# Optimization experiments

Hardware: AMD Instinct MI355X
Metric: run time of the kernel (lower is better)

## Reference

```python
import jax, jax.numpy as jnp
import numpy as np

V, E, H = 50000, 256, 512
BS, SEQ = 64, 200


def setup_inputs() -> dict:
    key = jax.random.key(0)
    ks = jax.random.split(key, 16)
    s = 0.05
    return {
        "input_idx": jax.random.randint(ks[0], (BS,), 0, V),
        "encoded": jax.random.normal(ks[1], (BS, SEQ, 2 * H), jnp.float32),
        "encoded_idx": jax.random.randint(ks[2], (BS, SEQ), 0, V),
        "prev_state": jax.random.normal(ks[3], (BS, H), jnp.float32),
        "weighted": jax.random.normal(ks[4], (BS, 1, 2 * H), jnp.float32),
        "order": 1,
        "embed_W": jax.random.normal(ks[5], (V, E), jnp.float32) * s,
        "Wih": jax.random.normal(ks[6], (3 * H, E + 2 * H), jnp.float32) * s,
        "Whh": jax.random.normal(ks[7], (3 * H, H), jnp.float32) * s,
        "bih": jax.random.normal(ks[8], (3 * H,), jnp.float32) * s,
        "bhh": jax.random.normal(ks[9], (3 * H,), jnp.float32) * s,
        "Ws_W": jax.random.normal(ks[10], (H, 2 * H), jnp.float32) * s,
        "Ws_b": jax.random.normal(ks[11], (H,), jnp.float32) * s,
        "Wo_W": jax.random.normal(ks[12], (V, H), jnp.float32) * s,
        "Wo_b": jax.random.normal(ks[13], (V,), jnp.float32) * s,
        "Wc_W": jax.random.normal(ks[14], (H, 2 * H), jnp.float32) * s,
        "Wc_b": jax.random.normal(ks[15], (H,), jnp.float32) * s,
    }


def reference(input_idx, encoded, encoded_idx, prev_state, weighted, order,
              embed_W, Wih, Whh, bih, bhh, Ws_W, Ws_b, Wo_W, Wo_b, Wc_W, Wc_b):
    bs, seq, _ = encoded.shape
    hidden = Ws_W.shape[0]
    vocab = Wo_W.shape[0]

    if order == 0:
        prev_state = encoded[:, 1] @ Ws_W.T + Ws_b            # [bs, H]
        weighted = jnp.zeros((bs, 1, 2 * hidden), encoded.dtype)

    # GRU single step (batch_first, seq len 1)
    x = jnp.concatenate([embed_W[input_idx], weighted[:, 0, :]], axis=1)  # [bs, E+2H]
    gi = x @ Wih.T + bih                                       # [bs, 3H]
    gh = prev_state @ Whh.T + bhh                              # [bs, 3H]
    i_r, i_z, i_n = jnp.split(gi, 3, axis=1)
    h_r, h_z, h_n = jnp.split(gh, 3, axis=1)
    r = jax.nn.sigmoid(i_r + h_r)
    z = jax.nn.sigmoid(i_z + h_z)
    n = jnp.tanh(i_n + r * h_n)
    state = (1.0 - z) * n + z * prev_state                     # [bs, H]

    # generate and copy scores
    score_g = state @ Wo_W.T + Wo_b                            # [bs, V]
    sc = jnp.tanh(encoded @ Wc_W.T + Wc_b)                     # [bs, seq, H]
    score_c = jnp.einsum('bsh,bh->bs', sc, state)              # [bs, seq]
    enc_mask = jnp.where(encoded_idx == 0, -1000.0, 0.0).astype(score_c.dtype)
    score_c = jnp.tanh(score_c + enc_mask)

    probs = jax.nn.softmax(jnp.concatenate([score_g, score_c], axis=1), axis=1)
    prob_g = probs[:, :vocab]                                  # [bs, V]
    prob_c = probs[:, vocab:]                                  # [bs, seq]

    # scatter-add copy probs into vocab slots
    prob_c_to_g = jnp.zeros((bs, vocab), probs.dtype).at[
        jnp.arange(bs)[:, None], encoded_idx].add(prob_c)
    out = (prob_g + prob_c_to_g)[:, None, :]                   # [bs, 1, V]

    # selective-read attention over positions matching input token
    m = (encoded_idx == input_idx[:, None]).astype(encoded.dtype)  # [bs, seq]
    ssum = m.sum(axis=1, keepdims=True)
    m = jnp.where(ssum > 1, m / ssum, m)
    attn = (prob_c * m)[:, None, :]                            # [bs, 1, seq]
    weighted_out = attn @ encoded                              # [bs, 1, 2H]

    return out, state, weighted_out
```

## Files before the change

### kernel.cpp

```cpp
#include <hip/hip_runtime.h>

#define V 50000
#define E_DIM 256
#define H_DIM 512
#define H2 1024
#define G3 1536
#define BSZ 64
#define SEQ 200
#define KX 1280
#define MROWS 12800
#define NBLK_WO 391

#define XBF_OFF   0
#define H0_OFF    40960
#define H0BF_OFF  73728
#define GI_OFF    90112
#define GH_OFF    188416
#define STBF_OFF  286720
#define WCBF_OFF  303104
#define SC_OFF    565248
#define REDG_OFF  590848
#define RED_OFF   690944

#define OUT_STATE 3200000
#define OUT_W     3232768

typedef __attribute__((ext_vector_type(8))) short bf16x8;
typedef __attribute__((ext_vector_type(4))) float f32x4;

__device__ __forceinline__ float sigmf(float x) { return 1.f / (1.f + __expf(-x)); }

__device__ __forceinline__ ushort f2bf(float f) {
  uint u = __float_as_uint(f);
  uint r = (u + 0x7FFFu + ((u >> 16) & 1u)) >> 16;
  return (ushort)r;
}

__device__ __forceinline__ float tanhfast(float x) {
  float xc = fminf(15.f, fmaxf(-15.f, x));
  float e = __expf(2.f * xc);
  return (e - 1.f) * __builtin_amdgcn_rcpf(e + 1.f);
}

__device__ __forceinline__ bf16x8 cvt8(float4 a, float4 b) {
  union { bf16x8 v; uint u[4]; } r;
  asm("v_cvt_pk_bf16_f32 %0, %1, %2" : "=v"(r.u[0]) : "v"(a.x), "v"(a.y));
  asm("v_cvt_pk_bf16_f32 %0, %1, %2" : "=v"(r.u[1]) : "v"(a.z), "v"(a.w));
  asm("v_cvt_pk_bf16_f32 %0, %1, %2" : "=v"(r.u[2]) : "v"(b.x), "v"(b.y));
  asm("v_cvt_pk_bf16_f32 %0, %1, %2" : "=v"(r.u[3]) : "v"(b.z), "v"(b.w));
  return r.v;
}

__device__ __forceinline__ void gload16(const void* g, void* l) {
  __builtin_amdgcn_global_load_lds(
      (__attribute__((address_space(1))) void*)(g),
      (__attribute__((address_space(3))) void*)(l), 16, 0, 0);
}

__global__ void kprep(const float* __restrict__ Wc_W, ushort* __restrict__ Wc_bf,
                      const int* __restrict__ input_idx, const float* __restrict__ encoded,
                      const float* __restrict__ prev_state, const float* __restrict__ weighted,
                      const int* __restrict__ order_p, const float* __restrict__ embed_W,
                      const float* __restrict__ Ws_W, const float* __restrict__ Ws_b,
                      ushort* __restrict__ x_bf, float* __restrict__ h0,
                      ushort* __restrict__ h0_bf) {
  int bid = blockIdx.x, tid = threadIdx.x;
  if (bid < 512) {
    int i = bid * 256 + tid;
    float4 v = ((const float4*)Wc_W)[i];
    ushort4 o;
    o.x = f2bf(v.x); o.y = f2bf(v.y); o.z = f2bf(v.z); o.w = f2bf(v.w);
    ((ushort4*)Wc_bf)[i] = o;
    return;
  }
  int b = bid - 512;
  int order = order_p[0];
  int idx = input_idx[b];
  x_bf[b * KX + tid] = f2bf(embed_W[(size_t)idx * E_DIM + tid]);
  if (order != 0) {
    for (int j = tid; j < H2; j += 256) x_bf[b * KX + E_DIM + j] = f2bf(weighted[b * H2 + j]);
    for (int j = tid; j < H_DIM; j += 256) {
      float v = prev_state[b * H_DIM + j];
      h0[b * H_DIM + j] = v;
      h0_bf[b * H_DIM + j] = f2bf(v);
    }
  } else {
    for (int j = tid; j < H2; j += 256) x_bf[b * KX + E_DIM + j] = 0;
    const float* er = encoded + ((size_t)b * SEQ + 1) * H2;
    for (int j = tid; j < H_DIM; j += 256) {
      float acc = Ws_b[j];
      const float* wr = Ws_W + (size_t)j * H2;
      for (int k = 0; k < H2; ++k) acc = fmaf(er[k], wr[k], acc);
      h0[b * H_DIM + j] = acc;
      h0_bf[b * H_DIM + j] = f2bf(acc);
    }
  }
}

__device__ __forceinline__ void gemm_small(const ushort* __restrict__ Abf,
                                           const float* __restrict__ W,
                                           const float* __restrict__ bias,
                                           float* __restrict__ out, int N, int kdim,
                                           int bid) {
  int tid = threadIdx.x;
  int lane = tid & 63, wv = tid >> 6;
  int l15 = lane & 15, lg = lane >> 4;
  int n0 = (bid * 4 + wv) * 16;
  int col = n0 + l15;
  bool valid = col < N;
  int colc = valid ? col : N - 1;
  f32x4 acc[4];
#pragma unroll
  for (int mt = 0; mt < 4; ++mt) acc[mt] = (f32x4){0.f, 0.f, 0.f, 0.f};
  const float* wrow = W + (size_t)colc * kdim + lg * 8;
  const ushort* arow = Abf + (size_t)l15 * kdim + lg * 8;
#pragma unroll 4
  for (int k0 = 0; k0 < kdim; k0 += 32) {
    float4 w0 = *(const float4*)(wrow + k0);
    float4 w1 = *(const float4*)(wrow + k0 + 4);
    bf16x8 bf = cvt8(w0, w1);
#pragma unroll
    for (int mt = 0; mt < 4; ++mt) {
      bf16x8 af = *(const bf16x8*)(arow + (size_t)mt * 16 * kdim + k0);
      acc[mt] = __builtin_amdgcn_mfma_f32_16x16x32_bf16(af, bf, acc[mt], 0, 0, 0);
    }
  }
  float bv = bias[colc];
  if (valid) {
#pragma unroll
    for (int mt = 0; mt < 4; ++mt)
#pragma unroll
      for (int r = 0; r < 4; ++r)
        out[(size_t)(mt * 16 + lg * 4 + r) * N + col] = acc[mt][r] + bv;
  }
}

__global__ __launch_bounds__(256) void mfma_gates(const ushort* __restrict__ x_bf,
                                                  const float* __restrict__ Wih,
                                                  const float* __restrict__ bih,
                                                  const ushort* __restrict__ h0_bf,
                                                  const float* __restrict__ Whh,
                                                  const float* __restrict__ bhh,
                                                  float* __restrict__ gi, float* __restrict__ gh) {
  if (blockIdx.y == 0)
    gemm_small(x_bf, Wih, bih, gi, G3, KX, blockIdx.x);
  else
    gemm_small(h0_bf, Whh, bhh, gh, G3, H_DIM, blockIdx.x);
}

__global__ void k2_gru(const float* __restrict__ gi, const float* __restrict__ gh,
                       const float* __restrict__ h0, float* __restrict__ state_out,
                       ushort* __restrict__ state_bf) {
  int b = blockIdx.x, j = threadIdx.x;
  float ir = gi[b * G3 + j], iz = gi[b * G3 + H_DIM + j], inn = gi[b * G3 + 2 * H_DIM + j];
  float hr = gh[b * G3 + j], hz = gh[b * G3 + H_DIM + j], hn = gh[b * G3 + 2 * H_DIM + j];
  float r = sigmf(ir + hr);
  float z = sigmf(iz + hz);
  float n = tanhf(inn + r * hn);
  float st = (1.f - z) * n + z * h0[b * H_DIM + j];
  state_out[b * H_DIM + j] = st;
  state_bf[b * H_DIM + j] = f2bf(st);
}

__global__ __launch_bounds__(256) void wo_stage(const ushort* __restrict__ state_bf,
                                                const float* __restrict__ Wo_W,
                                                const float* __restrict__ Wo_b,
                                                float* __restrict__ out,
                                                float* __restrict__ redg) {
  __shared__ char ldsW[2][16384];
  __shared__ float sm[4][64], ss[4][64];
  int tid = threadIdx.x, lane = tid & 63, wv = tid >> 6;
  int l15 = lane & 15, lg = lane >> 4;
  int bid = blockIdx.x;
  int c0 = bid * 128 + wv * 32;
  int col0 = c0 + l15, col1 = c0 + 16 + l15;
  int cc0 = col0 < V ? col0 : V - 1;
  int cc1 = col1 < V ? col1 : V - 1;
  const float* s0 = Wo_W + (size_t)cc0 * H_DIM + lg * 8;
  const float* s1 = Wo_W + (size_t)cc1 * H_DIM + lg * 8;
  const ushort* aptr = state_bf + (size_t)l15 * H_DIM + lg * 8;

  f32x4 acc[4][2];
#pragma unroll
  for (int mt = 0; mt < 4; ++mt)
#pragma unroll
    for (int nf = 0; nf < 2; ++nf) acc[mt][nf] = (f32x4){0.f, 0.f, 0.f, 0.f};

#define STGW(buf, it) do {                      \
    char* d_ = &ldsW[buf][wv * 4096];           \
    gload16(s0 + (it) * 32,     d_);            \
    gload16(s0 + (it) * 32 + 4, d_ + 1024);     \
    gload16(s1 + (it) * 32,     d_ + 2048);     \
    gload16(s1 + (it) * 32 + 4, d_ + 3072);     \
  } while (0)

  STGW(0, 0);
#pragma unroll 1
  for (int it = 0; it < 16; ++it) {
    int cur = it & 1;
    if (it < 15) {
      STGW(cur ^ 1, it + 1);
      asm volatile("s_waitcnt vmcnt(4)" ::: "memory");
    } else {
      asm volatile("s_waitcnt vmcnt(0)" ::: "memory");
    }
    const char* base = &ldsW[cur][wv * 4096];
    float4 w00 = *(const float4*)(base + lane * 16);
    float4 w01 = *(const float4*)(base + 1024 + lane * 16);
    float4 w10 = *(const float4*)(base + 2048 + lane * 16);
    float4 w11 = *(const float4*)(base + 3072 + lane * 16);
    bf16x8 wf0 = cvt8(w00, w01);
    bf16x8 wf1 = cvt8(w10, w11);
#pragma unroll
    for (int mt = 0; mt < 4; ++mt) {
      bf16x8 af = *(const bf16x8*)(aptr + (size_t)mt * 16 * H_DIM + it * 32);
      acc[mt][0] = __builtin_amdgcn_mfma_f32_16x16x32_bf16(af, wf0, acc[mt][0], 0, 0, 0);
      acc[mt][1] = __builtin_amdgcn_mfma_f32_16x16x32_bf16(af, wf1, acc[mt][1], 0, 0, 0);
    }
  }
#undef STGW

  float bv0 = Wo_b[cc0], bv1 = Wo_b[cc1];
  bool v0ok = col0 < V, v1ok = col1 < V;
#pragma unroll
  for (int mt = 0; mt < 4; ++mt)
#pragma unroll
    for (int r = 0; r < 4; ++r) {
      size_t row = (size_t)(mt * 16 + lg * 4 + r) * V;
      if (v0ok) out[row + col0] = acc[mt][0][r] + bv0;
      if (v1ok) out[row + col1] = acc[mt][1][r] + bv1;
    }
#pragma unroll
  for (int mt = 0; mt < 4; ++mt)
#pragma unroll
    for (int r = 0; r < 4; ++r) {
      float a0 = v0ok ? acc[mt][0][r] + bv0 : -1e30f;
      float a1 = v1ok ? acc[mt][1][r] + bv1 : -1e30f;
      float mx = fmaxf(a0, a1);
#pragma unroll
      for (int off = 1; off < 16; off <<= 1) mx = fmaxf(mx, __shfl_xor(mx, off, 64));
      float e = (v0ok ? __expf(a0 - mx) : 0.f) + (v1ok ? __expf(a1 - mx) : 0.f);
#pragma unroll
      for (int off = 1; off < 16; off <<= 1) e += __shfl_xor(e, off, 64);
      if (l15 == 0) {
        sm[wv][mt * 16 + lg * 4 + r] = mx;
        ss[wv][mt * 16 + lg * 4 + r] = e;
      }
    }
  __syncthreads();
  if (tid < 64) {
    float M = -1e30f, S = 0.f;
#pragma unroll
    for (int w = 0; w < 4; ++w) {
      float m2 = sm[w][tid], s2 = ss[w][tid];
      float mn = fmaxf(M, m2);
      S = S * __expf(M - mn) + s2 * __expf(m2 - mn);
      M = mn;
    }
    redg[((size_t)tid * NBLK_WO + bid) * 2] = M;
    redg[((size_t)tid * NBLK_WO + bid) * 2 + 1] = S;
  }
}

__global__ __launch_bounds__(256) void k4_mfma6(const float* __restrict__ encoded,
                                                const ushort* __restrict__ Wc_bf,
                                                const float* __restrict__ Wc_b,
                                                const float* __restrict__ state,
                                                float* __restrict__ scpart) {
  __shared__ char ldsA[2][16384];
  __shared__ float sred[4][64];
  int tid = threadIdx.x, lane = tid & 63, wv = tid >> 6;
  int l15 = lane & 15, lg = lane >> 4;
  int bid = blockIdx.x;
  int mtile = bid >> 1, nhalf = bid & 1;
  int m0 = mtile * 64;
  int nbase = nhalf * 256 + wv * 64;
  const float* sbase = encoded + (size_t)(m0 + wv * 16 + l15) * H2 + lg * 8;
  const ushort* bptr = Wc_bf + (size_t)(nbase + l15) * H2 + lg * 8;

  f32x4 acc[4][4];
#pragma unroll
  for (int mt = 0; mt < 4; ++mt)
#pragma unroll
    for (int nf = 0; nf < 4; ++nf) acc[mt][nf] = (f32x4){0.f, 0.f, 0.f, 0.f};

#define STG(buf, it) do {                       \
    const float* s_ = sbase + (it) * 64;        \
    char* d_ = &ldsA[buf][wv * 4096];           \
    gload16(s_,      d_);                       \
    gload16(s_ + 4,  d_ + 1024);                \
    gload16(s_ + 32, d_ + 2048);                \
    gload16(s_ + 36, d_ + 3072);                \
  } while (0)

  STG(0, 0);
#pragma unroll 1
  for (int it = 0; it < 16; ++it) {
    int cur = it & 1;
    __syncthreads();
    if (it < 15) STG(cur ^ 1, it + 1);
    const char* base = ldsA[cur];
#pragma unroll
    for (int khalf = 0; khalf < 2; ++khalf) {
      bf16x8 af[4];
#pragma unroll
      for (int mt = 0; mt < 4; ++mt) {
        float4 a0 = *(const float4*)(base + mt * 4096 + khalf * 2048 + lane * 16);
        float4 a1 = *(const float4*)(base + mt * 4096 + khalf * 2048 + 1024 + lane * 16);
        af[mt] = cvt8(a0, a1);
      }
#pragma unroll
      for (int nf = 0; nf < 4; ++nf) {
        bf16x8 bf = *(const bf16x8*)(bptr + (size_t)nf * 16 * H2 + it * 64 + khalf * 32);
#pragma unroll
        for (int mt = 0; mt < 4; ++mt)
          acc[mt][nf] = __builtin_amdgcn_mfma_f32_16x16x32_bf16(af[mt], bf, acc[mt][nf], 0, 0, 0);
      }
    }
  }
#undef STG

  float pv[4][4];
#pragma unroll
  for (int mt = 0; mt < 4; ++mt)
#pragma unroll
    for (int r = 0; r < 4; ++r) pv[mt][r] = 0.f;
#pragma unroll
  for (int nf = 0; nf < 4; ++nf) {
    int n = nbase + nf * 16 + l15;
    float bias = Wc_b[n];
#pragma unroll
    for (int mt = 0; mt < 4; ++mt) {
      int mrow = m0 + mt * 16 + lg * 4;
#pragma unroll
      for (int r = 0; r < 4; ++r) {
        int b = (mrow + r) / SEQ;
        pv[mt][r] += tanhfast(acc[mt][nf][r] + bias) * state[b * H_DIM + n];
      }
    }
  }
#pragma unroll
  for (int off = 1; off < 16; off <<= 1)
#pragma unroll
    for (int mt = 0; mt < 4; ++mt)
#pragma unroll
      for (int r = 0; r < 4; ++r) pv[mt][r] += __shfl_xor(pv[mt][r], off, 64);
  if (l15 == 0) {
#pragma unroll
    for (int mt = 0; mt < 4; ++mt)
#pragma unroll
      for (int r = 0; r < 4; ++r) sred[wv][mt * 16 + lg * 4 + r] = pv[mt][r];
  }
  __syncthreads();
  if (tid < 64) {
    float s = sred[0][tid] + sred[1][tid] + sred[2][tid] + sred[3][tid];
    scpart[(size_t)nhalf * MROWS + m0 + tid] = s;
  }
}

__global__ void kred(const float* __restrict__ redg, const float* __restrict__ scpart,
                     const int* __restrict__ eidx, float* __restrict__ red) {
  int b = blockIdx.x, tid = threadIdx.x;
  float m = -1e30f, s = 0.f;
  for (int i = tid; i < NBLK_WO; i += 256) {
    float m2 = redg[((size_t)b * NBLK_WO + i) * 2];
    float s2 = redg[((size_t)b * NBLK_WO + i) * 2 + 1];
    float mn = fmaxf(m, m2);
    s = s * __expf(m - mn) + s2 * __expf(m2 - mn);
    m = mn;
  }
  for (int i = tid; i < SEQ; i += 256) {
    int idx = b * SEQ + i;
    int ei = eidx[idx];
    float scv = scpart[idx] + scpart[MROWS + idx];
    float sc = tanhf(scv + (ei == 0 ? -1000.f : 0.f));
    float mn = fmaxf(m, sc);
    s = s * __expf(m - mn) + __expf(sc - mn);
    m = mn;
  }
  __shared__ float ms[256], ssh[256];
  ms[tid] = m; ssh[tid] = s;
  __syncthreads();
  for (int off = 128; off > 0; off >>= 1) {
    if (tid < off) {
      float m2 = ms[tid + off], s2 = ssh[tid + off];
      float mn = fmaxf(ms[tid], m2);
      ssh[tid] = ssh[tid] * __expf(ms[tid] - mn) + s2 * __expf(m2 - mn);
      ms[tid] = mn;
    }
    __syncthreads();
  }
  if (tid == 0) {
    red[b * 2] = ms[0];
    red[b * 2 + 1] = ssh[0];
  }
}

__global__ void k7_probs(float* __restrict__ sg, const float* __restrict__ red) {
  int i = blockIdx.x * 256 + threadIdx.x;
  int b = i / 12500;
  float mm = red[b * 2], rd = 1.f / red[b * 2 + 1];
  float4* p = (float4*)sg;
  float4 v = p[i];
  v.x = __expf(v.x - mm) * rd;
  v.y = __expf(v.y - mm) * rd;
  v.z = __expf(v.z - mm) * rd;
  v.w = __expf(v.w - mm) * rd;
  p[i] = v;
}

__global__ void k8_copy(const float* __restrict__ scpart, const int* __restrict__ eidx,
                        const int* __restrict__ input_idx, const float* __restrict__ red,
                        const float* __restrict__ encoded, float* __restrict__ out,
                        float* __restrict__ wout) {
  int b = blockIdx.x, tid = threadIdx.x;
  __shared__ float att_s[SEQ];
  __shared__ int cnt_s[256];
  float mm = red[b * 2], rd = 1.f / red[b * 2 + 1];
  int inp = input_idx[b];
  int cnt = 0;
  for (int s = tid; s < SEQ; s += 256) {
    int idx = b * SEQ + s;
    int ei = eidx[idx];
    float scv = scpart[idx] + scpart[MROWS + idx];
    float sc = tanhf(scv + (ei == 0 ? -1000.f : 0.f));
    float p = __expf(sc - mm) * rd;
    bool mt = (ei == inp);
    att_s[s] = mt ? p : 0.f;
    cnt += mt ? 1 : 0;
    atomicAdd(&out[(size_t)b * V + ei], p);
  }
  cnt_s[tid] = cnt;
  __syncthreads();
  for (int off = 128; off > 0; off >>= 1) {
    if (tid < off) cnt_s[tid] += cnt_s[tid + off];
    __syncthreads();
  }
  int c = cnt_s[0];
  float scale = (c > 1) ? 1.f / (float)c : 1.f;
  float w0 = 0, w1 = 0, w2 = 0, w3 = 0;
  for (int s = 0; s < SEQ; ++s) {
    float a = att_s[s];
    if (a != 0.f) {
      const float* er = encoded + ((size_t)b * SEQ + s) * H2;
      w0 += a * er[tid];
      w1 += a * er[tid + 256];
      w2 += a * er[tid + 512];
      w3 += a * er[tid + 768];
    }
  }
  wout[b * H2 + tid] = w0 * scale;
  wout[b * H2 + tid + 256] = w1 * scale;
  wout[b * H2 + tid + 512] = w2 * scale;
  wout[b * H2 + tid + 768] = w3 * scale;
}

extern "C" void kernel_launch(void* const* d_in, const int* in_sizes, int n_in,
                              void* d_out, int out_size, void* d_ws, size_t ws_size,
                              hipStream_t stream) {
  const int* input_idx = (const int*)d_in[0];
  const float* encoded = (const float*)d_in[1];
  const int* encoded_idx = (const int*)d_in[2];
  const float* prev_state = (const float*)d_in[3];
  const float* weighted = (const float*)d_in[4];
  const int* order_p = (const int*)d_in[5];
  const float* embed_W = (const float*)d_in[6];
  const float* Wih = (const float*)d_in[7];
  const float* Whh = (const float*)d_in[8];
  const float* bih = (const float*)d_in[9];
  const float* bhh = (const float*)d_in[10];
  const float* Ws_W = (const float*)d_in[11];
  const float* Ws_b = (const float*)d_in[12];
  const float* Wo_W = (const float*)d_in[13];
  const float* Wo_b = (const float*)d_in[14];
  const float* Wc_W = (const float*)d_in[15];
  const float* Wc_b = (const float*)d_in[16];

  float* ws = (float*)d_ws;
  float* out = (float*)d_out;
  ushort* x_bf = (ushort*)(ws + XBF_OFF);
  float* h0 = ws + H0_OFF;
  ushort* h0_bf = (ushort*)(ws + H0BF_OFF);
  float* gi = ws + GI_OFF;
  float* gh = ws + GH_OFF;
  ushort* state_bf = (ushort*)(ws + STBF_OFF);
  ushort* Wc_bf = (ushort*)(ws + WCBF_OFF);
  float* scpart = ws + SC_OFF;
  float* redg = ws + REDG_OFF;
  float* red = ws + RED_OFF;
  float* state = out + OUT_STATE;
  float* wout = out + OUT_W;

  kprep<<<576, 256, 0, stream>>>(Wc_W, Wc_bf, input_idx, encoded, prev_state, weighted,
                                 order_p, embed_W, Ws_W, Ws_b, x_bf, h0, h0_bf);
  mfma_gates<<<dim3(24, 2), 256, 0, stream>>>(x_bf, Wih, bih, h0_bf, Whh, bhh, gi, gh);
  k2_gru<<<64, 512, 0, stream>>>(gi, gh, h0, state, state_bf);
  wo_stage<<<NBLK_WO, 256, 0, stream>>>(state_bf, Wo_W, Wo_b, out, redg);
  k4_mfma6<<<400, 256, 0, stream>>>(encoded, Wc_bf, Wc_b, state, scpart);
  kred<<<64, 256, 0, stream>>>(redg, scpart, encoded_idx, red);
  k7_probs<<<3125, 256, 0, stream>>>(out, red);
  k8_copy<<<64, 256, 0, stream>>>(scpart, encoded_idx, input_idx, red, encoded, out, wout);
}
```

Before: 152.4 us.

## Deepen prefetch pipelines and retile encoded projection into per-wave quarter-N tiles

```diff
diff --git a/kernel.cpp b/kernel.cpp
--- a/kernel.cpp
+++ b/kernel.cpp
@@ -19,8 +19,8 @@
 #define STBF_OFF  286720
 #define WCBF_OFF  303104
 #define SC_OFF    565248
-#define REDG_OFF  590848
-#define RED_OFF   690944
+#define REDG_OFF  616448
+#define RED_OFF   666496
 
 #define OUT_STATE 3200000
 #define OUT_W     3232768
@@ -167,7 +167,7 @@
                                                 const float* __restrict__ Wo_b,
                                                 float* __restrict__ out,
                                                 float* __restrict__ redg) {
-  __shared__ char ldsW[2][16384];
+  __shared__ char ldsW[4][16384];
   __shared__ float sm[4][64], ss[4][64];
   int tid = threadIdx.x, lane = tid & 63, wv = tid >> 6;
   int l15 = lane & 15, lg = lane >> 4;
@@ -194,12 +194,16 @@
     gload16(s1 + (it) * 32 + 4, d_ + 3072);     \
   } while (0)
 
-  STGW(0, 0);
+  STGW(0, 0); STGW(1, 1); STGW(2, 2);
 #pragma unroll 1
   for (int it = 0; it < 16; ++it) {
-    int cur = it & 1;
-    if (it < 15) {
-      STGW(cur ^ 1, it + 1);
+    int cur = it & 3;
+    if (it < 13) {
+      STGW((it + 3) & 3, it + 3);
+      asm volatile("s_waitcnt vmcnt(12)" ::: "memory");
+    } else if (it == 13) {
+      asm volatile("s_waitcnt vmcnt(8)" ::: "memory");
+    } else if (it == 14) {
       asm volatile("s_waitcnt vmcnt(4)" ::: "memory");
     } else {
       asm volatile("s_waitcnt vmcnt(0)" ::: "memory");
@@ -262,99 +266,104 @@
   }
 }
 
-__global__ __launch_bounds__(256) void k4_mfma6(const float* __restrict__ encoded,
+__global__ __launch_bounds__(128) void k4_mfma7(const float* __restrict__ encoded,
                                                 const ushort* __restrict__ Wc_bf,
                                                 const float* __restrict__ Wc_b,
                                                 const float* __restrict__ state,
                                                 float* __restrict__ scpart) {
-  __shared__ char ldsA[2][16384];
-  __shared__ float sred[4][64];
+  __shared__ char ldsA[2][4][8192];
   int tid = threadIdx.x, lane = tid & 63, wv = tid >> 6;
   int l15 = lane & 15, lg = lane >> 4;
   int bid = blockIdx.x;
-  int mtile = bid >> 1, nhalf = bid & 1;
-  int m0 = mtile * 64;
-  int nbase = nhalf * 256 + wv * 64;
-  const float* sbase = encoded + (size_t)(m0 + wv * 16 + l15) * H2 + lg * 8;
-  const ushort* bptr = Wc_bf + (size_t)(nbase + l15) * H2 + lg * 8;
-
-  f32x4 acc[4][4];
-#pragma unroll
-  for (int mt = 0; mt < 4; ++mt)
-#pragma unroll
-    for (int nf = 0; nf < 4; ++nf) acc[mt][nf] = (f32x4){0.f, 0.f, 0.f, 0.f};
-
-#define STG(buf, it) do {                       \
-    const float* s_ = sbase + (it) * 64;        \
-    char* d_ = &ldsA[buf][wv * 4096];           \
-    gload16(s_,      d_);                       \
-    gload16(s_ + 4,  d_ + 1024);                \
-    gload16(s_ + 32, d_ + 2048);                \
-    gload16(s_ + 36, d_ + 3072);                \
+  int mgrp = bid >> 1;
+  int nq = (bid & 1) * 2 + wv;
+  int m0w = mgrp * 32;
+  int nbase = nq * 128;
+  const float* sbase = encoded + (size_t)m0w * H2;
+  const ushort* bbase = Wc_bf + (size_t)(nbase + l15) * H2 + lg * 8;
+
+  f32x4 acc[2][8];
+#pragma unroll
+  for (int mf = 0; mf < 2; ++mf)
+#pragma unroll
+    for (int nf = 0; nf < 8; ++nf) acc[mf][nf] = (f32x4){0.f, 0.f, 0.f, 0.f};
+
+#define STG(buf, it) do {                                                     \
+    char* d_ = &ldsA[wv][buf][0];                                             \
+    _Pragma("unroll") for (int ks = 0; ks < 2; ++ks)                          \
+    _Pragma("unroll") for (int mf = 0; mf < 2; ++mf)                          \
+    _Pragma("unroll") for (int h = 0; h < 2; ++h)                             \
+      gload16(sbase + (size_t)(mf * 16 + l15) * H2 + (it) * 64 + ks * 32 +    \
+                  h * 4 + lg * 8,                                             \
+              d_ + (((ks * 2 + mf) * 2 + h) * 64 + lane) * 16);               \
   } while (0)
 
-  STG(0, 0);
+  STG(0, 0); STG(1, 1); STG(2, 2);
 #pragma unroll 1
   for (int it = 0; it < 16; ++it) {
-    int cur = it & 1;
-    __syncthreads();
-    if (it < 15) STG(cur ^ 1, it + 1);
-    const char* base = ldsA[cur];
-#pragma unroll
-    for (int khalf = 0; khalf < 2; ++khalf) {
-      bf16x8 af[4];
-#pragma unroll
-      for (int mt = 0; mt < 4; ++mt) {
-        float4 a0 = *(const float4*)(base + mt * 4096 + khalf * 2048 + lane * 16);
-        float4 a1 = *(const float4*)(base + mt * 4096 + khalf * 2048 + 1024 + lane * 16);
-        af[mt] = cvt8(a0, a1);
+    int cur = it & 3;
+    if (it < 13) {
+      STG((it + 3) & 3, it + 3);
+      asm volatile("s_waitcnt vmcnt(24)" ::: "memory");
+    } else if (it == 13) {
+      asm volatile("s_waitcnt vmcnt(16)" ::: "memory");
+    } else if (it == 14) {
+      asm volatile("s_waitcnt vmcnt(8)" ::: "memory");
+    } else {
+      asm volatile("s_waitcnt vmcnt(0)" ::: "memory");
+    }
+    const char* base = &ldsA[wv][cur][0];
+#pragma unroll
+    for (int ks = 0; ks < 2; ++ks) {
+      bf16x8 af[2];
+#pragma unroll
+      for (int mf = 0; mf < 2; ++mf) {
+        float4 a0 = *(const float4*)(base + (((ks * 2 + mf) * 2 + 0) * 64 + lane) * 16);
+        float4 a1 = *(const float4*)(base + (((ks * 2 + mf) * 2 + 1) * 64 + lane) * 16);
+        af[mf] = cvt8(a0, a1);
       }
 #pragma unroll
-      for (int nf = 0; nf < 4; ++nf) {
-        bf16x8 bf = *(const bf16x8*)(bptr + (size_t)nf * 16 * H2 + it * 64 + khalf * 32);
-#pragma unroll
-        for (int mt = 0; mt < 4; ++mt)
-          acc[mt][nf] = __builtin_amdgcn_mfma_f32_16x16x32_bf16(af[mt], bf, acc[mt][nf], 0, 0, 0);
+      for (int nf = 0; nf < 8; ++nf) {
+        bf16x8 bf = *(const bf16x8*)(bbase + (size_t)nf * 16 * H2 + it * 64 + ks * 32);
+#pragma unroll
+        for (int mf = 0; mf < 2; ++mf)
+          acc[mf][nf] = __builtin_amdgcn_mfma_f32_16x16x32_bf16(af[mf], bf, acc[mf][nf], 0, 0, 0);
       }
     }
   }
 #undef STG
 
-  float pv[4][4];
-#pragma unroll
-  for (int mt = 0; mt < 4; ++mt)
-#pragma unroll
-    for (int r = 0; r < 4; ++r) pv[mt][r] = 0.f;
-#pragma unroll
-  for (int nf = 0; nf < 4; ++nf) {
+  float pv[2][4];
+#pragma unroll
+  for (int mf = 0; mf < 2; ++mf)
+#pragma unroll
+    for (int r = 0; r < 4; ++r) pv[mf][r] = 0.f;
+#pragma unroll
+  for (int nf = 0; nf < 8; ++nf) {
     int n = nbase + nf * 16 + l15;
     float bias = Wc_b[n];
 #pragma unroll
-    for (int mt = 0; mt < 4; ++mt) {
-      int mrow = m0 + mt * 16 + lg * 4;
+    for (int mf = 0; mf < 2; ++mf) {
+      int mrow = m0w + mf * 16 + lg * 4;
 #pragma unroll
       for (int r = 0; r < 4; ++r) {
         int b = (mrow + r) / SEQ;
-        pv[mt][r] += tanhfast(acc[mt][nf][r] + bias) * state[b * H_DIM + n];
+        pv[mf][r] += tanhfast(acc[mf][nf][r] + bias) * state[b * H_DIM + n];
       }
     }
   }
 #pragma unroll
   for (int off = 1; off < 16; off <<= 1)
 #pragma unroll
-    for (int mt = 0; mt < 4; ++mt)
-#pragma unroll
-      for (int r = 0; r < 4; ++r) pv[mt][r] += __shfl_xor(pv[mt][r], off, 64);
+    for (int mf = 0; mf < 2; ++mf)
+#pragma unroll
+      for (int r = 0; r < 4; ++r) pv[mf][r] += __shfl_xor(pv[mf][r], off, 64);
   if (l15 == 0) {
 #pragma unroll
-    for (int mt = 0; mt < 4; ++mt)
-#pragma unroll
-      for (int r = 0; r < 4; ++r) sred[wv][mt * 16 + lg * 4 + r] = pv[mt][r];
-  }
-  __syncthreads();
-  if (tid < 64) {
-    float s = sred[0][tid] + sred[1][tid] + sred[2][tid] + sred[3][tid];
-    scpart[(size_t)nhalf * MROWS + m0 + tid] = s;
+    for (int mf = 0; mf < 2; ++mf)
+#pragma unroll
+      for (int r = 0; r < 4; ++r)
+        scpart[(size_t)nq * MROWS + m0w + mf * 16 + lg * 4 + r] = pv[mf][r];
   }
 }
 
@@ -372,7 +381,8 @@
   for (int i = tid; i < SEQ; i += 256) {
     int idx = b * SEQ + i;
     int ei = eidx[idx];
-    float scv = scpart[idx] + scpart[MROWS + idx];
+    float scv = scpart[idx] + scpart[MROWS + idx] + scpart[2 * MROWS + idx] +
+                scpart[3 * MROWS + idx];
     float sc = tanhf(scv + (ei == 0 ? -1000.f : 0.f));
     float mn = fmaxf(m, sc);
     s = s * __expf(m - mn) + __expf(sc - mn);
@@ -422,7 +432,8 @@
   for (int s = tid; s < SEQ; s += 256) {
     int idx = b * SEQ + s;
     int ei = eidx[idx];
-    float scv = scpart[idx] + scpart[MROWS + idx];
+    float scv = scpart[idx] + scpart[MROWS + idx] + scpart[2 * MROWS + idx] +
+                scpart[3 * MROWS + idx];
     float sc = tanhf(scv + (ei == 0 ? -1000.f : 0.f));
     float p = __expf(sc - mm) * rd;
     bool mt = (ei == inp);
@@ -496,7 +507,7 @@
   mfma_gates<<<dim3(24, 2), 256, 0, stream>>>(x_bf, Wih, bih, h0_bf, Whh, bhh, gi, gh);
   k2_gru<<<64, 512, 0, stream>>>(gi, gh, h0, state, state_bf);
   wo_stage<<<NBLK_WO, 256, 0, stream>>>(state_bf, Wo_W, Wo_b, out, redg);
-  k4_mfma6<<<400, 256, 0, stream>>>(encoded, Wc_bf, Wc_b, state, scpart);
+  k4_mfma7<<<800, 128, 0, stream>>>(encoded, Wc_bf, Wc_b, state, scpart);
   kred<<<64, 256, 0, stream>>>(redg, scpart, encoded_idx, red);
   k7_probs<<<3125, 256, 0, stream>>>(out, red);
   k8_copy<<<64, 256, 0, stream>>>(scpart, encoded_idx, input_idx, red, encoded, out, wout);
```

Result: slower. 195.8 us (+28.5%).
